# Optimization experiments

Measured on AMD Instinct MI355X. Metric: run time of the kernel, lower is better.

## Reference

```python
import jax, jax.numpy as jnp
import numpy as np

LN_EPS = 1e-5  # torch LayerNorm default


def layer_norm(x, g, b):
    m = jnp.mean(x, axis=-1, keepdims=True)
    v = jnp.mean((x - m) ** 2, axis=-1, keepdims=True)
    return (x - m) / jnp.sqrt(v + LN_EPS) * g + b


def scatter_mean(src, idx, n):
    # src: [E, h], idx: [E] -> [n, h], mean with count clamped to >= 1
    s = jax.ops.segment_sum(src, idx, num_segments=n)
    cnt = jax.ops.segment_sum(jnp.ones((src.shape[0],), src.dtype), idx, num_segments=n)
    return s / jnp.clip(cnt, 1.0)[:, None]


def setup_inputs() -> dict:
    key = jax.random.key(0)
    ks = jax.random.split(key, 16)
    N, C, E, h = 200000, 50000, 600000, 128

    def w(k, shape, fan_in):
        return (jax.random.normal(k, shape, jnp.float32) / np.float32(np.sqrt(fan_in)))

    ci = jax.random.randint(ks[2], (E,), 0, C)
    vi = jax.random.randint(ks[3], (E,), 0, N)
    return {
        "vh": jax.random.normal(ks[0], (N, h), jnp.float32),
        "ch": jax.random.normal(ks[1], (C, h), jnp.float32),
        "edge_index": jnp.stack([ci, vi]).astype(jnp.int64),
        "ew": jax.random.normal(ks[4], (E,), jnp.float32),
        "v2c_lin_w": w(ks[5], (h, h), h), "v2c_lin_b": jnp.zeros((h,), jnp.float32),
        "v2c_gate_w": w(ks[6], (h, 1), 1), "v2c_gate_b": jnp.zeros((h,), jnp.float32),
        "v2c_upd_w": w(ks[7], (h, 2 * h), 2 * h), "v2c_upd_b": jnp.zeros((h,), jnp.float32),
        "v2c_ln_g": jnp.ones((h,), jnp.float32), "v2c_ln_b": jnp.zeros((h,), jnp.float32),
        "c2v_lin_w": w(ks[8], (h, h), h), "c2v_lin_b": jnp.zeros((h,), jnp.float32),
        "c2v_gate_w": w(ks[9], (h, 1), 1), "c2v_gate_b": jnp.zeros((h,), jnp.float32),
        "c2v_upd_w": w(ks[10], (h, 2 * h), 2 * h), "c2v_upd_b": jnp.zeros((h,), jnp.float32),
        "c2v_ln_g": jnp.ones((h,), jnp.float32), "c2v_ln_b": jnp.zeros((h,), jnp.float32),
    }


def reference(vh, ch, edge_index, ew,
              v2c_lin_w, v2c_lin_b, v2c_gate_w, v2c_gate_b,
              v2c_upd_w, v2c_upd_b, v2c_ln_g, v2c_ln_b,
              c2v_lin_w, c2v_lin_b, c2v_gate_w, c2v_gate_b,
              c2v_upd_w, c2v_upd_b, c2v_ln_g, c2v_ln_b):
    ci, vi = edge_index[0], edge_index[1]
    e = ew[:, None]  # [E, 1]

    # var -> con
    gate = jax.nn.sigmoid(e @ v2c_gate_w.T + v2c_gate_b)          # [E, h]
    msg = (vh @ v2c_lin_w.T + v2c_lin_b)[vi] * gate               # gather + gate
    agg = scatter_mean(msg, ci, ch.shape[0])                      # [C, h]
    ch_new = jax.nn.relu(layer_norm(
        jnp.concatenate([agg, ch], -1) @ v2c_upd_w.T + v2c_upd_b,
        v2c_ln_g, v2c_ln_b))

    # con -> var (uses updated ch)
    gate = jax.nn.sigmoid(e @ c2v_gate_w.T + c2v_gate_b)
    msg = (ch_new @ c2v_lin_w.T + c2v_lin_b)[ci] * gate
    agg = scatter_mean(msg, vi, vh.shape[0])                      # [N, h]
    vh_new = jax.nn.relu(layer_norm(
        jnp.concatenate([agg, vh], -1) @ c2v_upd_w.T + c2v_upd_b,
        c2v_ln_g, c2v_ln_b))

    return vh_new, ch_new
```

## Files before the change

### kernel.cpp

```cpp
#include <hip/hip_runtime.h>

#define LN_EPS 1e-5f

typedef float f32x4 __attribute__((ext_vector_type(4)));
typedef short bf16x8 __attribute__((ext_vector_type(8)));
typedef unsigned short u16x4 __attribute__((ext_vector_type(4)));

__device__ __forceinline__ unsigned short f2bf(float f) {
  unsigned int u = __float_as_uint(f);
  u = (u + 0x7fffu + ((u >> 16) & 1u)) >> 16;
  return (unsigned short)u;
}
__device__ __forceinline__ float bf2f(unsigned short h) {
  return __uint_as_float((unsigned int)h << 16);
}
__device__ __forceinline__ float sigm(float x) {
  return 1.f / (1.f + __expf(-x));
}

__global__ __launch_bounds__(256) void cvt_hist(const float* __restrict__ wa,
                                                const float* __restrict__ wb,
                                                const float* __restrict__ wc,
                                                const float* __restrict__ wd,
                                                unsigned short* __restrict__ oa,
                                                unsigned short* __restrict__ ob,
                                                unsigned short* __restrict__ oc,
                                                unsigned short* __restrict__ od,
                                                const int* __restrict__ ci,
                                                const int* __restrict__ vi,
                                                int* __restrict__ cntC,
                                                int* __restrict__ cntV,
                                                int* __restrict__ rankC,
                                                int* __restrict__ rankV, int E, int hgrid) {
  if ((int)blockIdx.x < 384) {
    int i = blockIdx.x * 256 + threadIdx.x;
    if (i < 16384) oa[i] = f2bf(wa[i]);
    else if (i < 49152) ob[i - 16384] = f2bf(wb[i - 16384]);
    else if (i < 65536) oc[i - 49152] = f2bf(wc[i - 49152]);
    else if (i < 98304) od[i - 65536] = f2bf(wd[i - 65536]);
    return;
  }
  int hb = blockIdx.x - 384;
  int tid = hb * 256 + threadIdx.x;
  int T = hgrid * 256;
  int e[8], c[8], v[8];
  bool ok[8];
#pragma unroll
  for (int i = 0; i < 8; ++i) {
    e[i] = tid + i * T;
    ok[i] = e[i] < E;
  }
#pragma unroll
  for (int i = 0; i < 8; ++i) if (ok[i]) c[i] = ci[e[i]];
#pragma unroll
  for (int i = 0; i < 8; ++i) if (ok[i]) v[i] = vi[e[i]];
  int rc[8], rv[8];
#pragma unroll
  for (int i = 0; i < 8; ++i) if (ok[i]) rc[i] = atomicAdd(&cntC[c[i]], 1);
#pragma unroll
  for (int i = 0; i < 8; ++i) if (ok[i]) rv[i] = atomicAdd(&cntV[v[i]], 1);
#pragma unroll
  for (int i = 0; i < 8; ++i) if (ok[i]) rankC[e[i]] = rc[i];
#pragma unroll
  for (int i = 0; i < 8; ++i) if (ok[i]) rankV[e[i]] = rv[i];
}

__device__ __forceinline__ void scan1_body(const int* __restrict__ cnt,
                                           int* __restrict__ off,
                                           int* __restrict__ bsum, int M, int bid,
                                           int* s) {
  int base = bid * 1024 + threadIdx.x * 4;
  int v[4];
  int tot = 0;
#pragma unroll
  for (int i = 0; i < 4; ++i) {
    int idx = base + i;
    v[i] = (idx < M) ? cnt[idx] : 0;
    tot += v[i];
  }
  s[threadIdx.x] = tot;
  __syncthreads();
  for (int d = 1; d < 256; d <<= 1) {
    int t = (threadIdx.x >= d) ? s[threadIdx.x - d] : 0;
    __syncthreads();
    s[threadIdx.x] += t;
    __syncthreads();
  }
  int excl = s[threadIdx.x] - tot;
#pragma unroll
  for (int i = 0; i < 4; ++i) {
    int idx = base + i;
    if (idx < M) off[idx] = excl;
    excl += v[i];
  }
  if (threadIdx.x == 255) bsum[bid] = s[255];
}

__global__ __launch_bounds__(256) void scanA(const int* __restrict__ cntC,
                                             int* __restrict__ offC,
                                             int* __restrict__ bsC, int Mc,
                                             const int* __restrict__ cntV,
                                             int* __restrict__ offV,
                                             int* __restrict__ bsV, int Mv, int nbC) {
  __shared__ int s[256];
  if ((int)blockIdx.x < nbC)
    scan1_body(cntC, offC, bsC, Mc, blockIdx.x, s);
  else
    scan1_body(cntV, offV, bsV, Mv, blockIdx.x - nbC, s);
}

__global__ __launch_bounds__(256) void scanB(int* __restrict__ bsC, int nbC,
                                             int* __restrict__ bsV, int nbV) {
  __shared__ int s[256];
  __shared__ int carry;
  int* bsum = (blockIdx.x == 0) ? bsC : bsV;
  int nb = (blockIdx.x == 0) ? nbC : nbV;
  if (threadIdx.x == 0) carry = 0;
  __syncthreads();
  for (int base = 0; base < nb; base += 256) {
    int idx = base + threadIdx.x;
    int v = (idx < nb) ? bsum[idx] : 0;
    s[threadIdx.x] = v;
    __syncthreads();
    for (int d = 1; d < 256; d <<= 1) {
      int t = (threadIdx.x >= d) ? s[threadIdx.x - d] : 0;
      __syncthreads();
      s[threadIdx.x] += t;
      __syncthreads();
    }
    if (idx < nb) bsum[idx] = s[threadIdx.x] - v + carry;
    __syncthreads();
    if (threadIdx.x == 0) carry += s[255];
    __syncthreads();
  }
}

__global__ __launch_bounds__(256) void scanC(int* __restrict__ offC,
                                             const int* __restrict__ bsC, int Mc,
                                             int* __restrict__ offV,
                                             const int* __restrict__ bsV, int Mv,
                                             int E, int gC) {
  if ((int)blockIdx.x < gC) {
    int idx = blockIdx.x * 256 + threadIdx.x;
    if (idx < Mc) offC[idx] += bsC[idx >> 10];
    if (idx == Mc) offC[Mc] = E;
  } else {
    int idx = (blockIdx.x - gC) * 256 + threadIdx.x;
    if (idx < Mv) offV[idx] += bsV[idx >> 10];
    if (idx == Mv) offV[Mv] = E;
  }
}

__global__ __launch_bounds__(512) void lin_scatter(
    const float* __restrict__ X, const unsigned short* __restrict__ Wbf,
    const float* __restrict__ bias, unsigned short* __restrict__ out,
    unsigned short* __restrict__ bfdst, int M,
    const int* __restrict__ ci, const int* __restrict__ vi,
    const float* __restrict__ ew, const int* __restrict__ offC,
    const int* __restrict__ offV, const int* __restrict__ rankC,
    const int* __restrict__ rankV, int2* __restrict__ edataC,
    int2* __restrict__ edataV, int E, int sgrid) {
  __shared__ unsigned short Bs[128][136];
  const int tid = threadIdx.x;
  const int bid = blockIdx.x;
  const int s3 = 3 * sgrid;

  bool isScatter;
  int sidx = 0, lidx;
  if (bid < s3) {
    if (bid % 3 == 0) {
      isScatter = true;
      sidx = bid / 3;
    } else {
      isScatter = false;
      lidx = bid - bid / 3 - 1;
    }
  } else {
    isScatter = false;
    lidx = bid - sgrid;
  }

  if (isScatter) {
    int gtid = sidx * 512 + tid;
    int T = sgrid * 512;
    int e[4], c[4], v[4], wb[4], rc[4], rv[4];
    bool ok[4];
#pragma unroll
    for (int i = 0; i < 4; ++i) {
      e[i] = gtid + i * T;
      ok[i] = e[i] < E;
    }
#pragma unroll
    for (int i = 0; i < 4; ++i) if (ok[i]) c[i] = ci[e[i]];
#pragma unroll
    for (int i = 0; i < 4; ++i) if (ok[i]) v[i] = vi[e[i]];
#pragma unroll
    for (int i = 0; i < 4; ++i) if (ok[i]) wb[i] = __float_as_int(ew[e[i]]);
#pragma unroll
    for (int i = 0; i < 4; ++i) if (ok[i]) rc[i] = rankC[e[i]];
#pragma unroll
    for (int i = 0; i < 4; ++i) if (ok[i]) rv[i] = rankV[e[i]];
#pragma unroll
    for (int i = 0; i < 4; ++i) if (ok[i]) edataC[offC[c[i]] + rc[i]] = make_int2(v[i], wb[i]);
#pragma unroll
    for (int i = 0; i < 4; ++i) if (ok[i]) edataV[offV[v[i]] + rv[i]] = make_int2(c[i], wb[i]);
    return;
  }

  const int lane = tid & 63, wv = tid >> 6;
  const int lr = lane & 15, lg = lane >> 4;
  const int row0 = lidx * 128 + wv * 16;
  const int arow = row0 + lr;
  const bool rowok = arow < M;
  const float* xrow = X + (size_t)arow * 128;

  float4 x0[4], x1[4];
#pragma unroll
  for (int ks = 0; ks < 4; ++ks) {
    int kb = ks * 32 + lg * 8;
    if (rowok) {
      x0[ks] = *reinterpret_cast<const float4*>(xrow + kb);
      x1[ks] = *reinterpret_cast<const float4*>(xrow + kb + 4);
    } else {
      x0[ks] = make_float4(0.f, 0.f, 0.f, 0.f);
      x1[ks] = x0[ks];
    }
  }

#pragma unroll
  for (int it = 0; it < 4; ++it) {
    int q = tid + it * 512;
    int n = q >> 4, kq = (q & 15) * 8;
    *reinterpret_cast<bf16x8*>(&Bs[n][kq]) =
        *reinterpret_cast<const bf16x8*>(&Wbf[(size_t)n * 128 + kq]);
  }

  bf16x8 a[4];
#pragma unroll
  for (int ks = 0; ks < 4; ++ks) {
    a[ks] = (bf16x8){(short)f2bf(x0[ks].x), (short)f2bf(x0[ks].y),
                     (short)f2bf(x0[ks].z), (short)f2bf(x0[ks].w),
                     (short)f2bf(x1[ks].x), (short)f2bf(x1[ks].y),
                     (short)f2bf(x1[ks].z), (short)f2bf(x1[ks].w)};
    if (rowok)
      *reinterpret_cast<bf16x8*>(&bfdst[(size_t)arow * 256 + 128 + ks * 32 + lg * 8]) = a[ks];
  }
  __syncthreads();

  f32x4 acc[8];
#pragma unroll
  for (int nf = 0; nf < 8; ++nf) acc[nf] = (f32x4)(0.f);
#pragma unroll
  for (int ks = 0; ks < 4; ++ks) {
#pragma unroll
    for (int nf = 0; nf < 8; ++nf) {
      bf16x8 b = *reinterpret_cast<const bf16x8*>(&Bs[nf * 16 + lr][ks * 32 + lg * 8]);
      acc[nf] = __builtin_amdgcn_mfma_f32_16x16x32_bf16(a[ks], b, acc[nf], 0, 0, 0);
    }
  }

#pragma unroll
  for (int nf = 0; nf < 8; ++nf) {
    int col = nf * 16 + lr;
    float bv = bias[col];
#pragma unroll
    for (int reg = 0; reg < 4; ++reg) {
      int grow = row0 + lg * 4 + reg;
      if (grow < M) out[(size_t)grow * 256 + col] = f2bf(acc[nf][reg] + bv);
    }
  }
}

__global__ __launch_bounds__(256) void seg_reduce(const int* __restrict__ off,
                                                  const int2* __restrict__ edata,
                                                  const float* __restrict__ gw,
                                                  const float* __restrict__ gb,
                                                  const unsigned short* __restrict__ src,
                                                  int srcStride,
                                                  unsigned short* __restrict__ out,
                                                  int outStride, int M) {
  int seg = blockIdx.x * 4 + (threadIdx.x >> 6);
  if (seg >= M) return;
  int j = threadIdx.x & 63;
  int start = off[seg], end = off[seg + 1];
  float gwa = gw[2 * j], gwb = gw[2 * j + 1];
  float gba = gb[2 * j], gbb = gb[2 * j + 1];
  float a0 = 0.f, a1 = 0.f;
  int p = start;
  for (; p + 4 <= end; p += 4) {
    int2 e0 = edata[p], e1 = edata[p + 1], e2 = edata[p + 2], e3 = edata[p + 3];
    unsigned int v0 = *reinterpret_cast<const unsigned int*>(&src[(size_t)e0.x * srcStride + 2 * j]);
    unsigned int v1 = *reinterpret_cast<const unsigned int*>(&src[(size_t)e1.x * srcStride + 2 * j]);
    unsigned int v2 = *reinterpret_cast<const unsigned int*>(&src[(size_t)e2.x * srcStride + 2 * j]);
    unsigned int v3 = *reinterpret_cast<const unsigned int*>(&src[(size_t)e3.x * srcStride + 2 * j]);
    float w0 = __int_as_float(e0.y), w1 = __int_as_float(e1.y);
    float w2 = __int_as_float(e2.y), w3 = __int_as_float(e3.y);
    a0 += bf2f((unsigned short)(v0 & 0xffff)) * sigm(w0 * gwa + gba)
        + bf2f((unsigned short)(v1 & 0xffff)) * sigm(w1 * gwa + gba)
        + bf2f((unsigned short)(v2 & 0xffff)) * sigm(w2 * gwa + gba)
        + bf2f((unsigned short)(v3 & 0xffff)) * sigm(w3 * gwa + gba);
    a1 += bf2f((unsigned short)(v0 >> 16)) * sigm(w0 * gwb + gbb)
        + bf2f((unsigned short)(v1 >> 16)) * sigm(w1 * gwb + gbb)
        + bf2f((unsigned short)(v2 >> 16)) * sigm(w2 * gwb + gbb)
        + bf2f((unsigned short)(v3 >> 16)) * sigm(w3 * gwb + gbb);
  }
  if (p + 2 <= end) {
    int2 e0 = edata[p], e1 = edata[p + 1];
    unsigned int v0 = *reinterpret_cast<const unsigned int*>(&src[(size_t)e0.x * srcStride + 2 * j]);
    unsigned int v1 = *reinterpret_cast<const unsigned int*>(&src[(size_t)e1.x * srcStride + 2 * j]);
    float w0 = __int_as_float(e0.y), w1 = __int_as_float(e1.y);
    a0 += bf2f((unsigned short)(v0 & 0xffff)) * sigm(w0 * gwa + gba)
        + bf2f((unsigned short)(v1 & 0xffff)) * sigm(w1 * gwa + gba);
    a1 += bf2f((unsigned short)(v0 >> 16)) * sigm(w0 * gwb + gbb)
        + bf2f((unsigned short)(v1 >> 16)) * sigm(w1 * gwb + gbb);
    p += 2;
  }
  if (p < end) {
    int2 e0 = edata[p];
    unsigned int v0 = *reinterpret_cast<const unsigned int*>(&src[(size_t)e0.x * srcStride + 2 * j]);
    float w0 = __int_as_float(e0.y);
    a0 += bf2f((unsigned short)(v0 & 0xffff)) * sigm(w0 * gwa + gba);
    a1 += bf2f((unsigned short)(v0 >> 16)) * sigm(w0 * gwb + gbb);
  }
  int cnt = end - start;
  float inv = 1.f / (float)(cnt > 1 ? cnt : 1);
  unsigned int packed = (unsigned int)f2bf(a0 * inv) | ((unsigned int)f2bf(a1 * inv) << 16);
  *reinterpret_cast<unsigned int*>(&out[(size_t)seg * outStride + 2 * j]) = packed;
}

__global__ __launch_bounds__(512) void gemm_lin_reg(const float* __restrict__ X,
                                                    const unsigned short* __restrict__ Wbf,
                                                    const float* __restrict__ bias,
                                                    unsigned short* __restrict__ out,
                                                    int M) {
  __shared__ unsigned short Bs[128][136];
  const int tid = threadIdx.x;
  const int lane = tid & 63, wv = tid >> 6;
  const int lr = lane & 15, lg = lane >> 4;
  const int row0 = blockIdx.x * 128 + wv * 16;
  const int arow = row0 + lr;
  const bool rowok = arow < M;
  const float* xrow = X + (size_t)arow * 128;

  float4 x0[4], x1[4];
#pragma unroll
  for (int ks = 0; ks < 4; ++ks) {
    int kb = ks * 32 + lg * 8;
    if (rowok) {
      x0[ks] = *reinterpret_cast<const float4*>(xrow + kb);
      x1[ks] = *reinterpret_cast<const float4*>(xrow + kb + 4);
    } else {
      x0[ks] = make_float4(0.f, 0.f, 0.f, 0.f);
      x1[ks] = x0[ks];
    }
  }
#pragma unroll
  for (int it = 0; it < 4; ++it) {
    int q = tid + it * 512;
    int n = q >> 4, kq = (q & 15) * 8;
    *reinterpret_cast<bf16x8*>(&Bs[n][kq]) =
        *reinterpret_cast<const bf16x8*>(&Wbf[(size_t)n * 128 + kq]);
  }
  bf16x8 a[4];
#pragma unroll
  for (int ks = 0; ks < 4; ++ks)
    a[ks] = (bf16x8){(short)f2bf(x0[ks].x), (short)f2bf(x0[ks].y),
                     (short)f2bf(x0[ks].z), (short)f2bf(x0[ks].w),
                     (short)f2bf(x1[ks].x), (short)f2bf(x1[ks].y),
                     (short)f2bf(x1[ks].z), (short)f2bf(x1[ks].w)};
  __syncthreads();

  f32x4 acc[8];
#pragma unroll
  for (int nf = 0; nf < 8; ++nf) acc[nf] = (f32x4)(0.f);
#pragma unroll
  for (int ks = 0; ks < 4; ++ks) {
#pragma unroll
    for (int nf = 0; nf < 8; ++nf) {
      bf16x8 b = *reinterpret_cast<const bf16x8*>(&Bs[nf * 16 + lr][ks * 32 + lg * 8]);
      acc[nf] = __builtin_amdgcn_mfma_f32_16x16x32_bf16(a[ks], b, acc[nf], 0, 0, 0);
    }
  }
#pragma unroll
  for (int nf = 0; nf < 8; ++nf) {
    int col = nf * 16 + lr;
    float bv = bias[col];
#pragma unroll
    for (int reg = 0; reg < 4; ++reg) {
      int grow = row0 + lg * 4 + reg;
      if (grow < M) out[(size_t)grow * 128 + col] = f2bf(acc[nf][reg] + bv);
    }
  }
}

template <bool CAT>
__global__ __launch_bounds__(512) void gemm_upd_reg(const unsigned short* __restrict__ Xa,
                                                    const float* __restrict__ base,
                                                    const unsigned short* __restrict__ Wbf,
                                                    const float* __restrict__ bias,
                                                    const float* __restrict__ lng,
                                                    const float* __restrict__ lnb,
                                                    float* __restrict__ out, int M) {
  __shared__ unsigned short Bs[128][136];
  const int tid = threadIdx.x;
  const int lane = tid & 63, wv = tid >> 6;
  const int lr = lane & 15, lg = lane >> 4;
  const int row0 = blockIdx.x * 128 + wv * 16;
  const int arow = row0 + lr;
  const bool rowok = arow < M;

  bf16x8 a[8];
  if constexpr (CAT) {
    const unsigned short* xr = Xa + (size_t)arow * 256;
#pragma unroll
    for (int ks = 0; ks < 8; ++ks)
      a[ks] = rowok ? *reinterpret_cast<const bf16x8*>(xr + ks * 32 + lg * 8) : (bf16x8)(short)0;
  } else {
    const unsigned short* ar = Xa + (size_t)arow * 128;
#pragma unroll
    for (int ks = 0; ks < 4; ++ks)
      a[ks] = rowok ? *reinterpret_cast<const bf16x8*>(ar + ks * 32 + lg * 8) : (bf16x8)(short)0;
    const float* br = base + (size_t)arow * 128;
#pragma unroll
    for (int ks = 4; ks < 8; ++ks) {
      float4 f0 = make_float4(0.f, 0.f, 0.f, 0.f), f1 = f0;
      if (rowok) {
        int kb = (ks - 4) * 32 + lg * 8;
        f0 = *reinterpret_cast<const float4*>(br + kb);
        f1 = *reinterpret_cast<const float4*>(br + kb + 4);
      }
      a[ks] = (bf16x8){(short)f2bf(f0.x), (short)f2bf(f0.y), (short)f2bf(f0.z), (short)f2bf(f0.w),
                       (short)f2bf(f1.x), (short)f2bf(f1.y), (short)f2bf(f1.z), (short)f2bf(f1.w)};
    }
  }

  bf16x8 wr[4];
  auto loadW = [&](int kh) {
#pragma unroll
    for (int it = 0; it < 4; ++it) {
      int q = tid + it * 512;
      int n = q >> 4, kq = (q & 15) * 8;
      wr[it] = *reinterpret_cast<const bf16x8*>(&Wbf[(size_t)n * 256 + kh * 128 + kq]);
    }
  };
  auto writeW = [&]() {
#pragma unroll
    for (int it = 0; it < 4; ++it) {
      int q = tid + it * 512;
      int n = q >> 4, kq = (q & 15) * 8;
      *reinterpret_cast<bf16x8*>(&Bs[n][kq]) = wr[it];
    }
  };

  f32x4 acc[8];
#pragma unroll
  for (int nf = 0; nf < 8; ++nf) acc[nf] = (f32x4)(0.f);

  loadW(0);
  writeW();
  __syncthreads();
  loadW(1);
#pragma unroll
  for (int ks = 0; ks < 4; ++ks) {
#pragma unroll
    for (int nf = 0; nf < 8; ++nf) {
      bf16x8 b = *reinterpret_cast<const bf16x8*>(&Bs[nf * 16 + lr][ks * 32 + lg * 8]);
      acc[nf] = __builtin_amdgcn_mfma_f32_16x16x32_bf16(a[ks], b, acc[nf], 0, 0, 0);
    }
  }
  __syncthreads();
  writeW();
  __syncthreads();
#pragma unroll
  for (int ks = 4; ks < 8; ++ks) {
#pragma unroll
    for (int nf = 0; nf < 8; ++nf) {
      bf16x8 b = *reinterpret_cast<const bf16x8*>(&Bs[nf * 16 + lr][(ks - 4) * 32 + lg * 8]);
      acc[nf] = __builtin_amdgcn_mfma_f32_16x16x32_bf16(a[ks], b, acc[nf], 0, 0, 0);
    }
  }

  float bv[8], gv[8], lv[8];
#pragma unroll
  for (int nf = 0; nf < 8; ++nf) {
    int col = nf * 16 + lr;
    bv[nf] = bias[col];
    gv[nf] = lng[col];
    lv[nf] = lnb[col];
  }
#pragma unroll
  for (int reg = 0; reg < 4; ++reg) {
    float z[8];
    float s = 0.f, q = 0.f;
#pragma unroll
    for (int nf = 0; nf < 8; ++nf) {
      z[nf] = acc[nf][reg] + bv[nf];
      s += z[nf];
      q += z[nf] * z[nf];
    }
#pragma unroll
    for (int m = 1; m < 16; m <<= 1) {
      s += __shfl_xor(s, m);
      q += __shfl_xor(q, m);
    }
    float mean = s * (1.f / 128.f);
    float var = q * (1.f / 128.f) - mean * mean;
    float rstd = rsqrtf(var + LN_EPS);
    int grow = row0 + lg * 4 + reg;
    if (grow < M) {
#pragma unroll
      for (int nf = 0; nf < 8; ++nf) {
        float y = (z[nf] - mean) * rstd * gv[nf] + lv[nf];
        out[(size_t)grow * 128 + nf * 16 + lr] = fmaxf(y, 0.f);
      }
    }
  }
}

extern "C" void kernel_launch(void* const* d_in, const int* in_sizes, int n_in,
                              void* d_out, int out_size, void* d_ws, size_t ws_size,
                              hipStream_t stream) {
  const float* vh = (const float*)d_in[0];
  const float* ch = (const float*)d_in[1];
  const int* ei = (const int*)d_in[2];
  const float* ew = (const float*)d_in[3];
  const float* v2c_lin_w = (const float*)d_in[4];
  const float* v2c_lin_b = (const float*)d_in[5];
  const float* v2c_gate_w = (const float*)d_in[6];
  const float* v2c_gate_b = (const float*)d_in[7];
  const float* v2c_upd_w = (const float*)d_in[8];
  const float* v2c_upd_b = (const float*)d_in[9];
  const float* v2c_ln_g = (const float*)d_in[10];
  const float* v2c_ln_b = (const float*)d_in[11];
  const float* c2v_lin_w = (const float*)d_in[12];
  const float* c2v_lin_b = (const float*)d_in[13];
  const float* c2v_gate_w = (const float*)d_in[14];
  const float* c2v_gate_b = (const float*)d_in[15];
  const float* c2v_upd_w = (const float*)d_in[16];
  const float* c2v_upd_b = (const float*)d_in[17];
  const float* c2v_ln_g = (const float*)d_in[18];
  const float* c2v_ln_b = (const float*)d_in[19];

  const int N = in_sizes[0] / 128;
  const int C = in_sizes[1] / 128;
  const int E = in_sizes[3];
  const int* ci = ei;
  const int* vi = ei + E;

  unsigned short* Xcat = (unsigned short*)d_ws;
  unsigned short* aggC = Xcat + (size_t)N * 256;
  unsigned short* wbf = aggC + (size_t)C * 128;
  unsigned short* wbfLinV = wbf;
  unsigned short* wbfUpdV = wbf + 16384;
  unsigned short* wbfLinC = wbf + 49152;
  unsigned short* wbfUpdC = wbf + 65536;
  int* offC = (int*)(wbf + 98304);
  int* offV = offC + (C + 1);
  size_t ofs = (size_t)((offV + (N + 1)) - (int*)d_ws);
  ofs = (ofs + 1) & ~(size_t)1;
  int2* edataC = (int2*)((int*)d_ws + ofs);
  int2* edataV = edataC + E;
  int* cntC = (int*)aggC;
  int* cntV = cntC + C;
  int* bsumC = cntV + N;
  int* bsumV = bsumC + 512;
  int* rankC = bsumV + 512;
  int* rankV = rankC + E;

  float* vhNew = (float*)d_out;
  float* chNew = (float*)d_out + (size_t)N * 128;

  const int hgrid = (E + 8 * 256 - 1) / (8 * 256);
  const int sgrid = (E + 4 * 512 - 1) / (4 * 512);
  const int nbC = (C + 1023) / 1024;
  const int nbN = (N + 1023) / 1024;
  const int gC = (C + 1 + 255) / 256;
  const int gN = (N + 1 + 255) / 256;

  hipMemsetAsync(cntC, 0, (size_t)(C + N) * sizeof(int), stream);
  cvt_hist<<<384 + hgrid, 256, 0, stream>>>(v2c_lin_w, v2c_upd_w, c2v_lin_w, c2v_upd_w,
                                            wbfLinV, wbfUpdV, wbfLinC, wbfUpdC,
                                            ci, vi, cntC, cntV, rankC, rankV, E, hgrid);

  scanA<<<nbC + nbN, 256, 0, stream>>>(cntC, offC, bsumC, C, cntV, offV, bsumV, N, nbC);
  scanB<<<2, 256, 0, stream>>>(bsumC, nbC, bsumV, nbN);
  scanC<<<gC + gN, 256, 0, stream>>>(offC, bsumC, C, offV, bsumV, N, E, gC);

  lin_scatter<<<sgrid + (N + 127) / 128, 512, 0, stream>>>(
      vh, wbfLinV, v2c_lin_b, Xcat, Xcat, N,
      ci, vi, ew, offC, offV, rankC, rankV, edataC, edataV, E, sgrid);

  seg_reduce<<<(C + 3) / 4, 256, 0, stream>>>(offC, edataC, v2c_gate_w, v2c_gate_b,
                                              Xcat, 256, aggC, 128, C);
  gemm_upd_reg<false><<<(C + 127) / 128, 512, 0, stream>>>(aggC, ch, wbfUpdV, v2c_upd_b,
                                                           v2c_ln_g, v2c_ln_b, chNew, C);

  unsigned short* tmpC = aggC;
  gemm_lin_reg<<<(C + 127) / 128, 512, 0, stream>>>(chNew, wbfLinC, c2v_lin_b, tmpC, C);
  seg_reduce<<<(N + 3) / 4, 256, 0, stream>>>(offV, edataV, c2v_gate_w, c2v_gate_b,
                                              tmpC, 128, Xcat, 256, N);
  gemm_upd_reg<true><<<(N + 127) / 128, 512, 0, stream>>>(Xcat, nullptr, wbfUpdC,
                                                          c2v_upd_b, c2v_ln_g, c2v_ln_b,
                                                          vhNew, N);
}
```

Baseline: 315.9 us.

## Fuse gated segment reduction into the update GEMM with LayerNorm

Merges the seg_reduce kernel into the update GEMM kernel. Each wave now reduces its 16 destination segments into a shared-memory tile, which then feeds the MFMA A operand directly. This removes the bf16 round trip of the aggregated features through global memory and two kernel launches. In exchange, the gather phase now runs at 512-thread, 128-row block granularity with extra LDS use, so there is less parallelism and occupancy for the latency-bound gather. Weight loads are issued early to overlap with it.

```diff
diff --git a/kernel.cpp b/kernel.cpp
--- a/kernel.cpp
+++ b/kernel.cpp
@@ -271,63 +271,6 @@
   }
 }
 
-__global__ __launch_bounds__(256) void seg_reduce(const int* __restrict__ off,
-                                                  const int2* __restrict__ edata,
-                                                  const float* __restrict__ gw,
-                                                  const float* __restrict__ gb,
-                                                  const unsigned short* __restrict__ src,
-                                                  int srcStride,
-                                                  unsigned short* __restrict__ out,
-                                                  int outStride, int M) {
-  int seg = blockIdx.x * 4 + (threadIdx.x >> 6);
-  if (seg >= M) return;
-  int j = threadIdx.x & 63;
-  int start = off[seg], end = off[seg + 1];
-  float gwa = gw[2 * j], gwb = gw[2 * j + 1];
-  float gba = gb[2 * j], gbb = gb[2 * j + 1];
-  float a0 = 0.f, a1 = 0.f;
-  int p = start;
-  for (; p + 4 <= end; p += 4) {
-    int2 e0 = edata[p], e1 = edata[p + 1], e2 = edata[p + 2], e3 = edata[p + 3];
-    unsigned int v0 = *reinterpret_cast<const unsigned int*>(&src[(size_t)e0.x * srcStride + 2 * j]);
-    unsigned int v1 = *reinterpret_cast<const unsigned int*>(&src[(size_t)e1.x * srcStride + 2 * j]);
-    unsigned int v2 = *reinterpret_cast<const unsigned int*>(&src[(size_t)e2.x * srcStride + 2 * j]);
-    unsigned int v3 = *reinterpret_cast<const unsigned int*>(&src[(size_t)e3.x * srcStride + 2 * j]);
-    float w0 = __int_as_float(e0.y), w1 = __int_as_float(e1.y);
-    float w2 = __int_as_float(e2.y), w3 = __int_as_float(e3.y);
-    a0 += bf2f((unsigned short)(v0 & 0xffff)) * sigm(w0 * gwa + gba)
-        + bf2f((unsigned short)(v1 & 0xffff)) * sigm(w1 * gwa + gba)
-        + bf2f((unsigned short)(v2 & 0xffff)) * sigm(w2 * gwa + gba)
-        + bf2f((unsigned short)(v3 & 0xffff)) * sigm(w3 * gwa + gba);
-    a1 += bf2f((unsigned short)(v0 >> 16)) * sigm(w0 * gwb + gbb)
-        + bf2f((unsigned short)(v1 >> 16)) * sigm(w1 * gwb + gbb)
-        + bf2f((unsigned short)(v2 >> 16)) * sigm(w2 * gwb + gbb)
-        + bf2f((unsigned short)(v3 >> 16)) * sigm(w3 * gwb + gbb);
-  }
-  if (p + 2 <= end) {
-    int2 e0 = edata[p], e1 = edata[p + 1];
-    unsigned int v0 = *reinterpret_cast<const unsigned int*>(&src[(size_t)e0.x * srcStride + 2 * j]);
-    unsigned int v1 = *reinterpret_cast<const unsigned int*>(&src[(size_t)e1.x * srcStride + 2 * j]);
-    float w0 = __int_as_float(e0.y), w1 = __int_as_float(e1.y);
-    a0 += bf2f((unsigned short)(v0 & 0xffff)) * sigm(w0 * gwa + gba)
-        + bf2f((unsigned short)(v1 & 0xffff)) * sigm(w1 * gwa + gba);
-    a1 += bf2f((unsigned short)(v0 >> 16)) * sigm(w0 * gwb + gbb)
-        + bf2f((unsigned short)(v1 >> 16)) * sigm(w1 * gwb + gbb);
-    p += 2;
-  }
-  if (p < end) {
-    int2 e0 = edata[p];
-    unsigned int v0 = *reinterpret_cast<const unsigned int*>(&src[(size_t)e0.x * srcStride + 2 * j]);
-    float w0 = __int_as_float(e0.y);
-    a0 += bf2f((unsigned short)(v0 & 0xffff)) * sigm(w0 * gwa + gba);
-    a1 += bf2f((unsigned short)(v0 >> 16)) * sigm(w0 * gwb + gbb);
-  }
-  int cnt = end - start;
-  float inv = 1.f / (float)(cnt > 1 ? cnt : 1);
-  unsigned int packed = (unsigned int)f2bf(a0 * inv) | ((unsigned int)f2bf(a1 * inv) << 16);
-  *reinterpret_cast<unsigned int*>(&out[(size_t)seg * outStride + 2 * j]) = packed;
-}
-
 __global__ __launch_bounds__(512) void gemm_lin_reg(const float* __restrict__ X,
                                                     const unsigned short* __restrict__ Wbf,
                                                     const float* __restrict__ bias,
@@ -394,13 +337,20 @@
 }
 
 template <bool CAT>
-__global__ __launch_bounds__(512) void gemm_upd_reg(const unsigned short* __restrict__ Xa,
-                                                    const float* __restrict__ base,
-                                                    const unsigned short* __restrict__ Wbf,
-                                                    const float* __restrict__ bias,
-                                                    const float* __restrict__ lng,
-                                                    const float* __restrict__ lnb,
-                                                    float* __restrict__ out, int M) {
+__global__ __launch_bounds__(512) void seg_upd(const int* __restrict__ off,
+                                               const int2* __restrict__ edata,
+                                               const float* __restrict__ gw,
+                                               const float* __restrict__ gb,
+                                               const unsigned short* __restrict__ src,
+                                               int srcStride,
+                                               const float* __restrict__ baseF,
+                                               const unsigned short* __restrict__ baseH,
+                                               const unsigned short* __restrict__ Wbf,
+                                               const float* __restrict__ bias,
+                                               const float* __restrict__ lng,
+                                               const float* __restrict__ lnb,
+                                               float* __restrict__ out, int M) {
+  __shared__ unsigned short Ag[128][136];
   __shared__ unsigned short Bs[128][136];
   const int tid = threadIdx.x;
   const int lane = tid & 63, wv = tid >> 6;
@@ -409,18 +359,85 @@
   const int arow = row0 + lr;
   const bool rowok = arow < M;
 
+  bf16x8 wr[4];
+  auto loadW = [&](int kh) {
+#pragma unroll
+    for (int it = 0; it < 4; ++it) {
+      int q = tid + it * 512;
+      int n = q >> 4, kq = (q & 15) * 8;
+      wr[it] = *reinterpret_cast<const bf16x8*>(&Wbf[(size_t)n * 256 + kh * 128 + kq]);
+    }
+  };
+  auto writeW = [&]() {
+#pragma unroll
+    for (int it = 0; it < 4; ++it) {
+      int q = tid + it * 512;
+      int n = q >> 4, kq = (q & 15) * 8;
+      *reinterpret_cast<bf16x8*>(&Bs[n][kq]) = wr[it];
+    }
+  };
+  loadW(0);
+
+  {
+    float gwa = gw[2 * lane], gwb = gw[2 * lane + 1];
+    float gba = gb[2 * lane], gbb = gb[2 * lane + 1];
+    for (int s = 0; s < 16; ++s) {
+      int seg = row0 + s;
+      if (seg >= M) break;
+      int start = off[seg], end = off[seg + 1];
+      float a0 = 0.f, a1 = 0.f;
+      int p = start;
+      for (; p + 4 <= end; p += 4) {
+        int2 e0 = edata[p], e1 = edata[p + 1], e2 = edata[p + 2], e3 = edata[p + 3];
+        unsigned int v0 = *reinterpret_cast<const unsigned int*>(&src[(size_t)e0.x * srcStride + 2 * lane]);
+        unsigned int v1 = *reinterpret_cast<const unsigned int*>(&src[(size_t)e1.x * srcStride + 2 * lane]);
+        unsigned int v2 = *reinterpret_cast<const unsigned int*>(&src[(size_t)e2.x * srcStride + 2 * lane]);
+        unsigned int v3 = *reinterpret_cast<const unsigned int*>(&src[(size_t)e3.x * srcStride + 2 * lane]);
+        float w0 = __int_as_float(e0.y), w1 = __int_as_float(e1.y);
+        float w2 = __int_as_float(e2.y), w3 = __int_as_float(e3.y);
+        a0 += bf2f((unsigned short)(v0 & 0xffff)) * sigm(w0 * gwa + gba)
+            + bf2f((unsigned short)(v1 & 0xffff)) * sigm(w1 * gwa + gba)
+            + bf2f((unsigned short)(v2 & 0xffff)) * sigm(w2 * gwa + gba)
+            + bf2f((unsigned short)(v3 & 0xffff)) * sigm(w3 * gwa + gba);
+        a1 += bf2f((unsigned short)(v0 >> 16)) * sigm(w0 * gwb + gbb)
+            + bf2f((unsigned short)(v1 >> 16)) * sigm(w1 * gwb + gbb)
+            + bf2f((unsigned short)(v2 >> 16)) * sigm(w2 * gwb + gbb)
+            + bf2f((unsigned short)(v3 >> 16)) * sigm(w3 * gwb + gbb);
+      }
+      if (p + 2 <= end) {
+        int2 e0 = edata[p], e1 = edata[p + 1];
+        unsigned int v0 = *reinterpret_cast<const unsigned int*>(&src[(size_t)e0.x * srcStride + 2 * lane]);
+        unsigned int v1 = *reinterpret_cast<const unsigned int*>(&src[(size_t)e1.x * srcStride + 2 * lane]);
+        float w0 = __int_as_float(e0.y), w1 = __int_as_float(e1.y);
+        a0 += bf2f((unsigned short)(v0 & 0xffff)) * sigm(w0 * gwa + gba)
+            + bf2f((unsigned short)(v1 & 0xffff)) * sigm(w1 * gwa + gba);
+        a1 += bf2f((unsigned short)(v0 >> 16)) * sigm(w0 * gwb + gbb)
+            + bf2f((unsigned short)(v1 >> 16)) * sigm(w1 * gwb + gbb);
+        p += 2;
+      }
+      if (p < end) {
+        int2 e0 = edata[p];
+        unsigned int v0 = *reinterpret_cast<const unsigned int*>(&src[(size_t)e0.x * srcStride + 2 * lane]);
+        float w0 = __int_as_float(e0.y);
+        a0 += bf2f((unsigned short)(v0 & 0xffff)) * sigm(w0 * gwa + gba);
+        a1 += bf2f((unsigned short)(v0 >> 16)) * sigm(w0 * gwb + gbb);
+      }
+      int cnt = end - start;
+      float inv = 1.f / (float)(cnt > 1 ? cnt : 1);
+      unsigned int packed = (unsigned int)f2bf(a0 * inv) | ((unsigned int)f2bf(a1 * inv) << 16);
+      *reinterpret_cast<unsigned int*>(&Ag[wv * 16 + s][2 * lane]) = packed;
+    }
+  }
+
   bf16x8 a[8];
   if constexpr (CAT) {
-    const unsigned short* xr = Xa + (size_t)arow * 256;
-#pragma unroll
-    for (int ks = 0; ks < 8; ++ks)
-      a[ks] = rowok ? *reinterpret_cast<const bf16x8*>(xr + ks * 32 + lg * 8) : (bf16x8)(short)0;
+#pragma unroll
+    for (int ks = 4; ks < 8; ++ks)
+      a[ks] = rowok ? *reinterpret_cast<const bf16x8*>(
+                          &baseH[(size_t)arow * 256 + 128 + (ks - 4) * 32 + lg * 8])
+                    : (bf16x8)(short)0;
   } else {
-    const unsigned short* ar = Xa + (size_t)arow * 128;
-#pragma unroll
-    for (int ks = 0; ks < 4; ++ks)
-      a[ks] = rowok ? *reinterpret_cast<const bf16x8*>(ar + ks * 32 + lg * 8) : (bf16x8)(short)0;
-    const float* br = base + (size_t)arow * 128;
+    const float* br = baseF + (size_t)arow * 128;
 #pragma unroll
     for (int ks = 4; ks < 8; ++ks) {
       float4 f0 = make_float4(0.f, 0.f, 0.f, 0.f), f1 = f0;
@@ -434,32 +451,17 @@
     }
   }
 
-  bf16x8 wr[4];
-  auto loadW = [&](int kh) {
-#pragma unroll
-    for (int it = 0; it < 4; ++it) {
-      int q = tid + it * 512;
-      int n = q >> 4, kq = (q & 15) * 8;
-      wr[it] = *reinterpret_cast<const bf16x8*>(&Wbf[(size_t)n * 256 + kh * 128 + kq]);
-    }
-  };
-  auto writeW = [&]() {
-#pragma unroll
-    for (int it = 0; it < 4; ++it) {
-      int q = tid + it * 512;
-      int n = q >> 4, kq = (q & 15) * 8;
-      *reinterpret_cast<bf16x8*>(&Bs[n][kq]) = wr[it];
-    }
-  };
-
-  f32x4 acc[8];
-#pragma unroll
-  for (int nf = 0; nf < 8; ++nf) acc[nf] = (f32x4)(0.f);
-
-  loadW(0);
+#pragma unroll
+  for (int ks = 0; ks < 4; ++ks)
+    a[ks] = *reinterpret_cast<const bf16x8*>(&Ag[wv * 16 + lr][ks * 32 + lg * 8]);
+
   writeW();
   __syncthreads();
   loadW(1);
+
+  f32x4 acc[8];
+#pragma unroll
+  for (int nf = 0; nf < 8; ++nf) acc[nf] = (f32x4)(0.f);
 #pragma unroll
   for (int ks = 0; ks < 4; ++ks) {
 #pragma unroll
@@ -548,8 +550,8 @@
   const int* vi = ei + E;
 
   unsigned short* Xcat = (unsigned short*)d_ws;
-  unsigned short* aggC = Xcat + (size_t)N * 256;
-  unsigned short* wbf = aggC + (size_t)C * 128;
+  unsigned short* tmpC = Xcat + (size_t)N * 256;
+  unsigned short* wbf = tmpC + (size_t)C * 128;
   unsigned short* wbfLinV = wbf;
   unsigned short* wbfUpdV = wbf + 16384;
   unsigned short* wbfLinC = wbf + 49152;
@@ -560,7 +562,7 @@
   ofs = (ofs + 1) & ~(size_t)1;
   int2* edataC = (int2*)((int*)d_ws + ofs);
   int2* edataV = edataC + E;
-  int* cntC = (int*)aggC;
+  int* cntC = (int*)tmpC;
   int* cntV = cntC + C;
   int* bsumC = cntV + N;
   int* bsumV = bsumC + 512;
@@ -590,16 +592,12 @@
       vh, wbfLinV, v2c_lin_b, Xcat, Xcat, N,
       ci, vi, ew, offC, offV, rankC, rankV, edataC, edataV, E, sgrid);
 
-  seg_reduce<<<(C + 3) / 4, 256, 0, stream>>>(offC, edataC, v2c_gate_w, v2c_gate_b,
-                                              Xcat, 256, aggC, 128, C);
-  gemm_upd_reg<false><<<(C + 127) / 128, 512, 0, stream>>>(aggC, ch, wbfUpdV, v2c_upd_b,
-                                                           v2c_ln_g, v2c_ln_b, chNew, C);
-
-  unsigned short* tmpC = aggC;
+  seg_upd<false><<<(C + 127) / 128, 512, 0, stream>>>(
+      offC, edataC, v2c_gate_w, v2c_gate_b, Xcat, 256, ch, nullptr,
+      wbfUpdV, v2c_upd_b, v2c_ln_g, v2c_ln_b, chNew, C);
+
   gemm_lin_reg<<<(C + 127) / 128, 512, 0, stream>>>(chNew, wbfLinC, c2v_lin_b, tmpC, C);
-  seg_reduce<<<(N + 3) / 4, 256, 0, stream>>>(offV, edataV, c2v_gate_w, c2v_gate_b,
-                                              tmpC, 128, Xcat, 256, N);
-  gemm_upd_reg<true><<<(N + 127) / 128, 512, 0, stream>>>(Xcat, nullptr, wbfUpdC,
-                                                          c2v_upd_b, c2v_ln_g, c2v_ln_b,
-                                                          vhNew, N);
-}
+  seg_upd<true><<<(N + 127) / 128, 512, 0, stream>>>(
+      offV, edataV, c2v_gate_w, c2v_gate_b, tmpC, 128, nullptr, Xcat,
+      wbfUpdC, c2v_upd_b, c2v_ln_g, c2v_ln_b, vhNew, N);
+}
```

Result: slower. 350.7 us (+11.0%).
